# Kernel optimization log

Hardware: AMD Instinct MI355X
Metric: run time of the kernel (lower is better)

The kernel has to match this reference:

```python
import jax, jax.numpy as jnp
import numpy as np

N_HEAD = 16
D_K = 64
D_MODEL = N_HEAD * D_K
LN_EPS = 1e-5


def setup_inputs() -> dict:
    key = jax.random.key(0)
    ks = jax.random.split(key, 11)
    B, Tq, Tk = 4, 2048, 2048
    s = 1.0 / np.sqrt(D_MODEL)
    return {
        "q": jax.random.normal(ks[0], (B, Tq, D_MODEL), jnp.float32),
        "k": jax.random.normal(ks[1], (B, Tk, D_MODEL), jnp.float32),
        "v": jax.random.normal(ks[2], (B, Tk, D_MODEL), jnp.float32),
        "Wq": jax.random.normal(ks[3], (D_MODEL, D_MODEL), jnp.float32) * s,
        "bq": jnp.zeros((D_MODEL,), jnp.float32),
        "Wk": jax.random.normal(ks[4], (D_MODEL, D_MODEL), jnp.float32) * s,
        "bk": jnp.zeros((D_MODEL,), jnp.float32),
        "Wv": jax.random.normal(ks[5], (D_MODEL, D_MODEL), jnp.float32) * s,
        "bv": jnp.zeros((D_MODEL,), jnp.float32),
        "Wo": jax.random.normal(ks[6], (D_MODEL, D_MODEL), jnp.float32) * s,
        "bo": jnp.zeros((D_MODEL,), jnp.float32),
        "gamma": jnp.ones((D_MODEL,), jnp.float32),
        "beta": jnp.zeros((D_MODEL,), jnp.float32),
    }


def reference(q, k, v, Wq, bq, Wk, bk, Wv, bv, Wo, bo, gamma, beta):
    B, Tq, _ = q.shape
    Tk = k.shape[1]
    temperature = jnp.asarray(D_K ** 0.5, q.dtype)

    # projections (torch Linear: x @ W.T + b), reshape to heads: [B, T, H, DK]
    qh = (q @ Wq.T + bq).reshape(B, Tq, N_HEAD, D_K)
    kh = (k @ Wk.T + bk).reshape(B, Tk, N_HEAD, D_K)
    vh = (v @ Wv.T + bv).reshape(B, Tk, N_HEAD, D_K)

    # scores [B, H, Tq, Tk]; softmax over Tk (dropout is identity in eval)
    scores = jnp.einsum('bqhd,bkhd->bhqk', qh, kh) / temperature
    attn = jax.nn.softmax(scores, axis=-1)

    # attention output -> concat heads [B, Tq, D_MODEL]
    out = jnp.einsum('bhqk,bkhd->bqhd', attn, vh).reshape(B, Tq, D_MODEL)

    out = out @ Wo.T + bo
    x = out + q  # residual
    mu = jnp.mean(x, axis=-1, keepdims=True)
    var = jnp.var(x, axis=-1, keepdims=True)
    out_norm = (x - mu) * jax.lax.rsqrt(var + LN_EPS) * gamma + beta

    # attn returned in torch layout [NHead*B, Tq, Tk]
    attn_flat = attn.transpose(1, 0, 2, 3).reshape(N_HEAD * B, Tq, Tk)
    return (out_norm, attn_flat)
```

## Files before the change

### kernel.cpp

```cpp
#include <hip/hip_runtime.h>
#include <cstdint>
#include <cstddef>

typedef __attribute__((ext_vector_type(4))) float f32x4;
typedef __attribute__((ext_vector_type(8))) short s16x8;
typedef __attribute__((ext_vector_type(4))) unsigned short u16x4;
typedef __attribute__((ext_vector_type(8))) unsigned short u16x8;

#define MFMA16(a, b, c) __builtin_amdgcn_mfma_f32_16x16x32_bf16((a), (b), (c), 0, 0, 0)
#define GLOAD_LDS16(src, dst)                                             \
  __builtin_amdgcn_global_load_lds(                                       \
      (const __attribute__((address_space(1))) void*)(src),               \
      (__attribute__((address_space(3))) void*)(dst), 16, 0, 0)

static constexpr int kD = 1024;
static constexpr int kT = 2048;

__device__ __forceinline__ unsigned short f2bf(float f) {
  union { float f; uint32_t u; } v; v.f = f;
  uint32_t r = v.u + 0x7fffu + ((v.u >> 16) & 1u);
  return (unsigned short)(r >> 16);
}
__device__ __forceinline__ float bf2f(unsigned short h) {
  union { float f; uint32_t u; } v; v.u = ((uint32_t)h) << 16;
  return v.f;
}

__global__ __launch_bounds__(256) void convert_all_k(
    const float* __restrict__ q, const float* __restrict__ k,
    const float* __restrict__ v, const float* __restrict__ Wq,
    const float* __restrict__ Wk, const float* __restrict__ Wv,
    const float* __restrict__ Wo, unsigned short* __restrict__ q_hi,
    unsigned short* __restrict__ q_lo, unsigned short* __restrict__ k_hi,
    unsigned short* __restrict__ k_lo, unsigned short* __restrict__ v_b,
    unsigned short* __restrict__ Wq_hi, unsigned short* __restrict__ Wq_lo,
    unsigned short* __restrict__ Wk_hi, unsigned short* __restrict__ Wk_lo,
    unsigned short* __restrict__ Wv_b, unsigned short* __restrict__ Wo_b) {
  constexpr int nq4 = (4 * 2048 * 1024) / 4;
  constexpr int nw4 = (1024 * 1024) / 4;
  constexpr int total = 3 * nq4 + 4 * nw4;
  for (int i = blockIdx.x * 256 + threadIdx.x; i < total; i += gridDim.x * 256) {
    const float* src;
    unsigned short *hi, *lo = nullptr;
    int off;
    if (i < nq4) { src = q; hi = q_hi; lo = q_lo; off = i; }
    else if (i < 2 * nq4) { src = k; hi = k_hi; lo = k_lo; off = i - nq4; }
    else if (i < 3 * nq4) { src = v; hi = v_b; off = i - 2 * nq4; }
    else if (i < 3 * nq4 + nw4) { src = Wq; hi = Wq_hi; lo = Wq_lo; off = i - 3 * nq4; }
    else if (i < 3 * nq4 + 2 * nw4) { src = Wk; hi = Wk_hi; lo = Wk_lo; off = i - 3 * nq4 - nw4; }
    else if (i < 3 * nq4 + 3 * nw4) { src = Wv; hi = Wv_b; off = i - 3 * nq4 - 2 * nw4; }
    else { src = Wo; hi = Wo_b; off = i - 3 * nq4 - 3 * nw4; }
    f32x4 vv = ((const f32x4*)src)[off];
    u16x4 h4, l4;
#pragma unroll
    for (int j = 0; j < 4; j++) {
      h4[j] = f2bf(vv[j]);
      l4[j] = f2bf(vv[j] - bf2f(h4[j]));
    }
    ((u16x4*)hi)[off] = h4;
    if (lo) ((u16x4*)lo)[off] = l4;
  }
}

template <int MODE, int MINW>
__global__ __launch_bounds__(256, MINW) void gemm_bf16(
    const unsigned short* __restrict__ Xhi, const unsigned short* __restrict__ Xlo,
    const unsigned short* __restrict__ Whi, const unsigned short* __restrict__ Wlo,
    const float* __restrict__ bias, const float* __restrict__ resid,
    unsigned short* __restrict__ outB, float* __restrict__ outF, float oscale) {
  constexpr bool SPLIT = (MODE == 0);
  __shared__ unsigned short smem[(SPLIT ? 4 : 2) * 128 * 64];
  unsigned short* Ah = smem;
  unsigned short* Bh = smem + 8192;
  unsigned short* Al = SPLIT ? smem + 16384 : smem;
  unsigned short* Bl = SPLIT ? smem + 24576 : smem;

  const int tid = threadIdx.x, lane = tid & 63, w = tid >> 6;
  const int wg = (blockIdx.x & 7) * 64 + (blockIdx.x >> 3);
  const int m0 = (wg >> 3) * 128, n0 = (wg & 7) * 128;
  const int wm0 = (w >> 1) * 64, wn0 = (w & 1) * 64;
  const int lr = lane & 15, lk = lane >> 4;
  const int srow = lane >> 3, sslot = (lane & 7) ^ srow;

  const size_t xoff = (size_t)(m0 + w * 32 + srow) * kD + sslot * 8;
  const size_t woff = (size_t)(n0 + w * 32 + srow) * kD + sslot * 8;

  f32x4 acc[4][4];
#pragma unroll
  for (int i = 0; i < 4; i++)
#pragma unroll
    for (int j = 0; j < 4; j++) acc[i][j] = (f32x4){0.f, 0.f, 0.f, 0.f};

  for (int kt = 0; kt < kD / 64; ++kt) {
    __syncthreads();
    const int kof = kt * 64;
#pragma unroll
    for (int i = 0; i < 4; i++) {
      const int ldst = (w * 32 + i * 8) * 64;
      GLOAD_LDS16(Xhi + xoff + (size_t)i * 8 * kD + kof, &Ah[ldst]);
      GLOAD_LDS16(Whi + woff + (size_t)i * 8 * kD + kof, &Bh[ldst]);
      if constexpr (SPLIT) {
        GLOAD_LDS16(Xlo + xoff + (size_t)i * 8 * kD + kof, &Al[ldst]);
        GLOAD_LDS16(Wlo + woff + (size_t)i * 8 * kD + kof, &Bl[ldst]);
      }
    }
    __syncthreads();
#pragma unroll
    for (int ks = 0; ks < 2; ks++) {
      s16x8 af[4], bf[4], al[4], bl[4];
#pragma unroll
      for (int i = 0; i < 4; i++) {
        const int ra = wm0 + i * 16 + lr;
        const int oa = ra * 128 + ((((ks * 4) + lk) ^ (ra & 7)) << 4);
        const int rb = wn0 + i * 16 + lr;
        const int ob = rb * 128 + ((((ks * 4) + lk) ^ (rb & 7)) << 4);
        af[i] = *(const s16x8*)((const char*)Ah + oa);
        bf[i] = *(const s16x8*)((const char*)Bh + ob);
        if constexpr (SPLIT) {
          al[i] = *(const s16x8*)((const char*)Al + oa);
          bl[i] = *(const s16x8*)((const char*)Bl + ob);
        }
      }
#pragma unroll
      for (int i = 0; i < 4; i++)
#pragma unroll
        for (int j = 0; j < 4; j++) {
          if constexpr (SPLIT) {
            acc[i][j] = MFMA16(al[i], bf[j], acc[i][j]);
            acc[i][j] = MFMA16(af[i], bl[j], acc[i][j]);
          }
          acc[i][j] = MFMA16(af[i], bf[j], acc[i][j]);
        }
    }
  }

#pragma unroll
  for (int j = 0; j < 4; j++) {
    const int col = n0 + wn0 + j * 16 + lr;
    const float bv = bias[col];
#pragma unroll
    for (int i = 0; i < 4; i++)
#pragma unroll
      for (int r = 0; r < 4; r++) {
        const int row = m0 + wm0 + i * 16 + lk * 4 + r;
        const size_t idx = (size_t)row * kD + col;
        float vv = acc[i][j][r] + bv;
        if constexpr (MODE == 0) {
          outB[idx] = f2bf(vv * oscale);
        } else if constexpr (MODE == 1) {
          outB[idx] = f2bf(vv);
        } else {
          outF[idx] = vv + resid[idx];
        }
      }
  }
}

__global__ __launch_bounds__(256) void transpose_v(
    const unsigned short* __restrict__ vh, unsigned short* __restrict__ vhT) {
  __shared__ unsigned short lds[64 * 72];
  const int bx = blockIdx.x;
  const int tt = bx & 31, bhp = bx >> 5;
  const int b = bhp >> 4, h = bhp & 15;
  const int t0 = tt * 64, tid = threadIdx.x;
  {
    const int t = tid >> 2, c0 = (tid & 3) * 16;
    const unsigned short* src = &vh[(size_t)(b * kT + t0 + t) * kD + h * 64 + c0];
    u16x8 v0 = *(const u16x8*)src;
    u16x8 v1 = *(const u16x8*)(src + 8);
    *(u16x8*)&lds[t * 72 + c0] = v0;
    *(u16x8*)&lds[t * 72 + c0 + 8] = v1;
  }
  __syncthreads();
  {
    const int d = tid >> 2, tc0 = (tid & 3) * 16;
    u16x8 o0, o1;
#pragma unroll
    for (int i = 0; i < 8; i++) o0[i] = lds[(tc0 + i) * 72 + d];
#pragma unroll
    for (int i = 0; i < 8; i++) o1[i] = lds[(tc0 + 8 + i) * 72 + d];
    size_t base = ((size_t)((b * 16 + h) * 64 + d)) * kT + t0 + tc0;
    *(u16x8*)&vhT[base] = o0;
    *(u16x8*)&vhT[base + 8] = o1;
  }
}

__global__ __launch_bounds__(256, 2) void attn_fused(
    const unsigned short* __restrict__ qh, const unsigned short* __restrict__ kh,
    const unsigned short* __restrict__ vhT, unsigned short* __restrict__ attn_out,
    float* __restrict__ attn_p) {
  __shared__ unsigned short kbuf[2][64 * 64];
  __shared__ unsigned short vbuf[2][64 * 64];
  __shared__ unsigned short qp[9216];

  const int tid = threadIdx.x, lane = tid & 63, w = tid >> 6;
  const int lr = lane & 15, lk = lane >> 4;
  const int srow = lane >> 3, sslot = (lane & 7) ^ srow;
  const int wg = (blockIdx.x & 7) * 128 + (blockIdx.x >> 3);
  const int bh = wg >> 4, qt = wg & 15;
  const int h = bh >> 2, b = bh & 3;
  const int q0 = qt * 128, qm0 = w * 32;

  const size_t qsrc = (size_t)(b * kT + q0 + w * 32 + srow) * kD + h * 64 + sslot * 8;
#pragma unroll
  for (int i = 0; i < 4; i++)
    GLOAD_LDS16(qh + qsrc + (size_t)i * 8 * kD, &qp[(w * 32 + i * 8) * 64]);

  const size_t kbase = (size_t)(b * kT + w * 16 + srow) * kD + h * 64 + sslot * 8;
  const size_t vbase = ((size_t)((b * 16 + h) * 64) + w * 16 + srow) * kT + sslot * 8;

#pragma unroll
  for (int i = 0; i < 2; i++)
    GLOAD_LDS16(kh + kbase + (size_t)(i * 8) * kD, &kbuf[0][(w * 16 + i * 8) * 64]);
  __syncthreads();

  s16x8 qf[2][2];
#pragma unroll
  for (int mq = 0; mq < 2; mq++)
#pragma unroll
    for (int ks = 0; ks < 2; ks++) {
      const int rq = qm0 + mq * 16 + lr;
      qf[mq][ks] = *(const s16x8*)((const char*)qp + rq * 128 +
                                   ((((ks * 4) + lk) ^ (rq & 7)) << 4));
    }

  float l_part[2] = {0.f, 0.f};

  for (int kt = 0; kt < kT / 64; ++kt) {
    if (kt + 1 < kT / 64) {
#pragma unroll
      for (int i = 0; i < 2; i++)
        GLOAD_LDS16(kh + kbase + (size_t)((kt + 1) * 64 + i * 8) * kD,
                    &kbuf[(kt + 1) & 1][(w * 16 + i * 8) * 64]);
    }
    const unsigned short* kb = kbuf[kt & 1];
    f32x4 sc[2][4];
#pragma unroll
    for (int mq = 0; mq < 2; mq++)
#pragma unroll
      for (int ni = 0; ni < 4; ni++) sc[mq][ni] = (f32x4){0.f, 0.f, 0.f, 0.f};
#pragma unroll
    for (int ks = 0; ks < 2; ks++) {
      s16x8 kf[4];
#pragma unroll
      for (int ni = 0; ni < 4; ni++) {
        const int rk = ni * 16 + lr;
        kf[ni] = *(const s16x8*)((const char*)kb + rk * 128 +
                                 ((((ks * 4) + lk) ^ (rk & 7)) << 4));
      }
#pragma unroll
      for (int mq = 0; mq < 2; mq++)
#pragma unroll
        for (int ni = 0; ni < 4; ni++)
          sc[mq][ni] = MFMA16(kf[ni], qf[mq][ks], sc[mq][ni]);
    }
#pragma unroll
    for (int mq = 0; mq < 2; mq++)
#pragma unroll
      for (int ni = 0; ni < 4; ni++)
        l_part[mq] += __expf(sc[mq][ni][0]) + __expf(sc[mq][ni][1]) +
                      __expf(sc[mq][ni][2]) + __expf(sc[mq][ni][3]);
    __syncthreads();
  }

  float rl[2];
#pragma unroll
  for (int mq = 0; mq < 2; mq++) {
    float s = l_part[mq];
    s += __shfl_xor(s, 16, 64);
    s += __shfl_xor(s, 32, 64);
    rl[mq] = 1.0f / s;
  }

  f32x4 pv[2][4];
#pragma unroll
  for (int mq = 0; mq < 2; mq++)
#pragma unroll
    for (int nd = 0; nd < 4; nd++) pv[mq][nd] = (f32x4){0.f, 0.f, 0.f, 0.f};

#pragma unroll
  for (int i = 0; i < 2; i++) {
    const int ldst = (w * 16 + i * 8) * 64;
    GLOAD_LDS16(kh + kbase + (size_t)(i * 8) * kD, &kbuf[0][ldst]);
    GLOAD_LDS16(vhT + vbase + (size_t)i * 8 * kT, &vbuf[0][ldst]);
  }
  unsigned short* p_w = &qp[w * 2304];
  __syncthreads();

  for (int kt = 0; kt < kT / 64; ++kt) {
    if (kt + 1 < kT / 64) {
#pragma unroll
      for (int i = 0; i < 2; i++) {
        const int ldst = (w * 16 + i * 8) * 64;
        GLOAD_LDS16(kh + kbase + (size_t)((kt + 1) * 64 + i * 8) * kD,
                    &kbuf[(kt + 1) & 1][ldst]);
        GLOAD_LDS16(vhT + vbase + (size_t)i * 8 * kT + (kt + 1) * 64,
                    &vbuf[(kt + 1) & 1][ldst]);
      }
    }
    const unsigned short* kb = kbuf[kt & 1];
    const unsigned short* vb = vbuf[kt & 1];
    f32x4 sc[2][4];
#pragma unroll
    for (int mq = 0; mq < 2; mq++)
#pragma unroll
      for (int ni = 0; ni < 4; ni++) sc[mq][ni] = (f32x4){0.f, 0.f, 0.f, 0.f};
#pragma unroll
    for (int ks = 0; ks < 2; ks++) {
      s16x8 kf[4];
#pragma unroll
      for (int ni = 0; ni < 4; ni++) {
        const int rk = ni * 16 + lr;
        kf[ni] = *(const s16x8*)((const char*)kb + rk * 128 +
                                 ((((ks * 4) + lk) ^ (rk & 7)) << 4));
      }
#pragma unroll
      for (int mq = 0; mq < 2; mq++)
#pragma unroll
        for (int ni = 0; ni < 4; ni++)
          sc[mq][ni] = MFMA16(kf[ni], qf[mq][ks], sc[mq][ni]);
    }
#pragma unroll
    for (int mq = 0; mq < 2; mq++) {
      const int qrow = q0 + qm0 + mq * 16 + lr;
      float* prow = attn_p + ((size_t)(bh * kT + qrow)) * kT + kt * 64 + 4 * lk;
#pragma unroll
      for (int ni = 0; ni < 4; ni++) {
        f32x4 pr;
#pragma unroll
        for (int r = 0; r < 4; r++) pr[r] = __expf(sc[mq][ni][r]) * rl[mq];
        __builtin_nontemporal_store(pr, (f32x4*)(prow + ni * 16));
        uint32_t d0, d1;
        asm("v_cvt_pk_bf16_f32 %0, %1, %2" : "=v"(d0) : "v"(pr[0]), "v"(pr[1]));
        asm("v_cvt_pk_bf16_f32 %0, %1, %2" : "=v"(d1) : "v"(pr[2]), "v"(pr[3]));
        uint2 dd; dd.x = d0; dd.y = d1;
        *(uint2*)&p_w[(mq * 16 + lr) * 72 + ni * 16 + 4 * lk] = dd;
      }
    }
#pragma unroll
    for (int ks = 0; ks < 2; ks++) {
      s16x8 pf[2], vf[4];
#pragma unroll
      for (int mq = 0; mq < 2; mq++)
        pf[mq] = *(const s16x8*)&p_w[(mq * 16 + lr) * 72 + ks * 32 + lk * 8];
#pragma unroll
      for (int nd = 0; nd < 4; nd++) {
        const int row = nd * 16 + lr;
        const int sw2 = ((ks * 4) + lk) ^ (row & 7);
        vf[nd] = *(const s16x8*)((const char*)vb + row * 128 + (sw2 << 4));
      }
#pragma unroll
      for (int mq = 0; mq < 2; mq++)
#pragma unroll
        for (int nd = 0; nd < 4; nd++)
          pv[mq][nd] = MFMA16(pf[mq], vf[nd], pv[mq][nd]);
    }
    __syncthreads();
  }

#pragma unroll
  for (int mq = 0; mq < 2; mq++)
#pragma unroll
    for (int nd = 0; nd < 4; nd++)
#pragma unroll
      for (int r = 0; r < 4; r++) {
        const int qrow = q0 + qm0 + mq * 16 + lk * 4 + r;
        attn_out[((size_t)(b * kT + qrow)) * kD + h * 64 + nd * 16 + lr] =
            f2bf(pv[mq][nd][r]);
      }
}

__global__ __launch_bounds__(256) void ln_kernel(
    const float* __restrict__ x, const float* __restrict__ gamma,
    const float* __restrict__ beta, float* __restrict__ out) {
  __shared__ float ssum[4], ssq[4];
  const int row = blockIdx.x, tid = threadIdx.x;
  f32x4 v = *(const f32x4*)&x[(size_t)row * kD + tid * 4];
  float s = v[0] + v[1] + v[2] + v[3];
  float q2 = v[0] * v[0] + v[1] * v[1] + v[2] * v[2] + v[3] * v[3];
#pragma unroll
  for (int d = 1; d < 64; d <<= 1) {
    s += __shfl_xor(s, d, 64);
    q2 += __shfl_xor(q2, d, 64);
  }
  const int w = tid >> 6, lane = tid & 63;
  if (lane == 0) {
    ssum[w] = s;
    ssq[w] = q2;
  }
  __syncthreads();
  s = ssum[0] + ssum[1] + ssum[2] + ssum[3];
  q2 = ssq[0] + ssq[1] + ssq[2] + ssq[3];
  const float mu = s * (1.f / 1024.f);
  const float var = q2 * (1.f / 1024.f) - mu * mu;
  const float rstd = rsqrtf(var + 1e-5f);
  f32x4 g = *(const f32x4*)&gamma[tid * 4];
  f32x4 bb = *(const f32x4*)&beta[tid * 4];
  f32x4 o;
#pragma unroll
  for (int j = 0; j < 4; j++) o[j] = (v[j] - mu) * rstd * g[j] + bb[j];
  *(f32x4*)&out[(size_t)row * kD + tid * 4] = o;
}

extern "C" void kernel_launch(void* const* d_in, const int* in_sizes, int n_in,
                              void* d_out, int out_size, void* d_ws,
                              size_t ws_size, hipStream_t stream) {
  const float* q = (const float*)d_in[0];
  const float* k = (const float*)d_in[1];
  const float* v = (const float*)d_in[2];
  const float* Wq = (const float*)d_in[3];
  const float* bq = (const float*)d_in[4];
  const float* Wk = (const float*)d_in[5];
  const float* bk = (const float*)d_in[6];
  const float* Wv = (const float*)d_in[7];
  const float* bv = (const float*)d_in[8];
  const float* Wo = (const float*)d_in[9];
  const float* bo = (const float*)d_in[10];
  const float* gamma = (const float*)d_in[11];
  const float* beta = (const float*)d_in[12];

  float* out = (float*)d_out;
  float* attn_p = out + (size_t)8192 * 1024;

  constexpr size_t NQ = (size_t)4 * 2048 * 1024;
  constexpr size_t NW = (size_t)1024 * 1024;

  unsigned short* w16 = (unsigned short*)d_ws;
  unsigned short* q_hi = w16 + 0 * NQ;
  unsigned short* q_lo = w16 + 1 * NQ;
  unsigned short* k_hi = w16 + 2 * NQ;
  unsigned short* k_lo = w16 + 3 * NQ;
  unsigned short* v_b  = w16 + 4 * NQ;
  unsigned short* qh_b = w16 + 5 * NQ;
  unsigned short* kh_b = w16 + 6 * NQ;
  unsigned short* vh_b = w16 + 7 * NQ;
  unsigned short* vhT  = w16 + 8 * NQ;
  unsigned short* ao_b = w16 + 9 * NQ;
  unsigned short* Wq_hi = w16 + 10 * NQ;
  unsigned short* Wq_lo = Wq_hi + NW;
  unsigned short* Wk_hi = Wq_hi + 2 * NW;
  unsigned short* Wk_lo = Wq_hi + 3 * NW;
  unsigned short* Wv_b  = Wq_hi + 4 * NW;
  unsigned short* Wo_b  = Wq_hi + 5 * NW;
  float* xbuf = (float*)(Wq_hi + 6 * NW);

  dim3 blk(256);
  convert_all_k<<<2048, blk, 0, stream>>>(q, k, v, Wq, Wk, Wv, Wo, q_hi, q_lo,
                                          k_hi, k_lo, v_b, Wq_hi, Wq_lo, Wk_hi,
                                          Wk_lo, Wv_b, Wo_b);

  gemm_bf16<0, 2><<<512, blk, 0, stream>>>(q_hi, q_lo, Wq_hi, Wq_lo, bq, nullptr,
                                           qh_b, nullptr, 0.125f);
  gemm_bf16<0, 2><<<512, blk, 0, stream>>>(k_hi, k_lo, Wk_hi, Wk_lo, bk, nullptr,
                                           kh_b, nullptr, 1.0f);
  gemm_bf16<1, 3><<<512, blk, 0, stream>>>(v_b, nullptr, Wv_b, nullptr, bv, nullptr,
                                           vh_b, nullptr, 1.0f);
  transpose_v<<<2048, blk, 0, stream>>>(vh_b, vhT);
  attn_fused<<<1024, blk, 0, stream>>>(qh_b, kh_b, vhT, ao_b, attn_p);
  gemm_bf16<2, 3><<<512, blk, 0, stream>>>(ao_b, nullptr, Wo_b, nullptr, bo, q,
                                           nullptr, xbuf, 1.0f);
  ln_kernel<<<8192, blk, 0, stream>>>(xbuf, gamma, beta, out);
}
```

Before: 555.7 us.

## Replace split-bf16 Q/K projections with single-pass fp16 MFMA

The Q and K projections used a hi/lo bf16 split costing three MFMAs per tile plus extra conversion traffic and LDS. They now convert inputs and weights once to fp16, run one fp16 MFMA pass, and store qh/kh as fp16 so the QK^T scores in attention also use fp16 MFMA. This drops the lo buffers, halves projection MFMA work and cuts the bytes the convert kernel writes. Attention occupancy is raised to 3 waves. The trade-off is relying on fp16's extra mantissa bits instead of the split for score accuracy, with some overflow risk if activations are large.

```diff
diff --git a/kernel.cpp b/kernel.cpp
--- a/kernel.cpp
+++ b/kernel.cpp
@@ -4,10 +4,12 @@
 
 typedef __attribute__((ext_vector_type(4))) float f32x4;
 typedef __attribute__((ext_vector_type(8))) short s16x8;
+typedef __attribute__((ext_vector_type(8))) _Float16 f16x8;
 typedef __attribute__((ext_vector_type(4))) unsigned short u16x4;
 typedef __attribute__((ext_vector_type(8))) unsigned short u16x8;
 
-#define MFMA16(a, b, c) __builtin_amdgcn_mfma_f32_16x16x32_bf16((a), (b), (c), 0, 0, 0)
+#define MFMA_BF16(a, b, c) __builtin_amdgcn_mfma_f32_16x16x32_bf16((a), (b), (c), 0, 0, 0)
+#define MFMA_F16(a, b, c) __builtin_amdgcn_mfma_f32_16x16x32_f16((a), (b), (c), 0, 0, 0)
 #define GLOAD_LDS16(src, dst)                                             \
   __builtin_amdgcn_global_load_lds(                                       \
       (const __attribute__((address_space(1))) void*)(src),               \
@@ -21,59 +23,51 @@
   uint32_t r = v.u + 0x7fffu + ((v.u >> 16) & 1u);
   return (unsigned short)(r >> 16);
 }
-__device__ __forceinline__ float bf2f(unsigned short h) {
-  union { float f; uint32_t u; } v; v.u = ((uint32_t)h) << 16;
-  return v.f;
+__device__ __forceinline__ unsigned short f2h(float f) {
+  union { _Float16 h; unsigned short u; } cv;
+  cv.h = (_Float16)f;
+  return cv.u;
 }
 
 __global__ __launch_bounds__(256) void convert_all_k(
     const float* __restrict__ q, const float* __restrict__ k,
     const float* __restrict__ v, const float* __restrict__ Wq,
     const float* __restrict__ Wk, const float* __restrict__ Wv,
-    const float* __restrict__ Wo, unsigned short* __restrict__ q_hi,
-    unsigned short* __restrict__ q_lo, unsigned short* __restrict__ k_hi,
-    unsigned short* __restrict__ k_lo, unsigned short* __restrict__ v_b,
-    unsigned short* __restrict__ Wq_hi, unsigned short* __restrict__ Wq_lo,
-    unsigned short* __restrict__ Wk_hi, unsigned short* __restrict__ Wk_lo,
+    const float* __restrict__ Wo, unsigned short* __restrict__ q_h,
+    unsigned short* __restrict__ k_h, unsigned short* __restrict__ v_b,
+    unsigned short* __restrict__ Wq_h, unsigned short* __restrict__ Wk_h,
     unsigned short* __restrict__ Wv_b, unsigned short* __restrict__ Wo_b) {
   constexpr int nq4 = (4 * 2048 * 1024) / 4;
   constexpr int nw4 = (1024 * 1024) / 4;
   constexpr int total = 3 * nq4 + 4 * nw4;
   for (int i = blockIdx.x * 256 + threadIdx.x; i < total; i += gridDim.x * 256) {
     const float* src;
-    unsigned short *hi, *lo = nullptr;
+    unsigned short* dst;
     int off;
-    if (i < nq4) { src = q; hi = q_hi; lo = q_lo; off = i; }
-    else if (i < 2 * nq4) { src = k; hi = k_hi; lo = k_lo; off = i - nq4; }
-    else if (i < 3 * nq4) { src = v; hi = v_b; off = i - 2 * nq4; }
-    else if (i < 3 * nq4 + nw4) { src = Wq; hi = Wq_hi; lo = Wq_lo; off = i - 3 * nq4; }
-    else if (i < 3 * nq4 + 2 * nw4) { src = Wk; hi = Wk_hi; lo = Wk_lo; off = i - 3 * nq4 - nw4; }
-    else if (i < 3 * nq4 + 3 * nw4) { src = Wv; hi = Wv_b; off = i - 3 * nq4 - 2 * nw4; }
-    else { src = Wo; hi = Wo_b; off = i - 3 * nq4 - 3 * nw4; }
+    bool use_f16;
+    if (i < nq4) { src = q; dst = q_h; off = i; use_f16 = true; }
+    else if (i < 2 * nq4) { src = k; dst = k_h; off = i - nq4; use_f16 = true; }
+    else if (i < 3 * nq4) { src = v; dst = v_b; off = i - 2 * nq4; use_f16 = false; }
+    else if (i < 3 * nq4 + nw4) { src = Wq; dst = Wq_h; off = i - 3 * nq4; use_f16 = true; }
+    else if (i < 3 * nq4 + 2 * nw4) { src = Wk; dst = Wk_h; off = i - 3 * nq4 - nw4; use_f16 = true; }
+    else if (i < 3 * nq4 + 3 * nw4) { src = Wv; dst = Wv_b; off = i - 3 * nq4 - 2 * nw4; use_f16 = false; }
+    else { src = Wo; dst = Wo_b; off = i - 3 * nq4 - 3 * nw4; use_f16 = false; }
     f32x4 vv = ((const f32x4*)src)[off];
-    u16x4 h4, l4;
-#pragma unroll
-    for (int j = 0; j < 4; j++) {
-      h4[j] = f2bf(vv[j]);
-      l4[j] = f2bf(vv[j] - bf2f(h4[j]));
-    }
-    ((u16x4*)hi)[off] = h4;
-    if (lo) ((u16x4*)lo)[off] = l4;
-  }
-}
-
-template <int MODE, int MINW>
-__global__ __launch_bounds__(256, MINW) void gemm_bf16(
-    const unsigned short* __restrict__ Xhi, const unsigned short* __restrict__ Xlo,
-    const unsigned short* __restrict__ Whi, const unsigned short* __restrict__ Wlo,
+    u16x4 o4;
+#pragma unroll
+    for (int j = 0; j < 4; j++) o4[j] = use_f16 ? f2h(vv[j]) : f2bf(vv[j]);
+    ((u16x4*)dst)[off] = o4;
+  }
+}
+
+template <int MODE>
+__global__ __launch_bounds__(256, 3) void gemm_16(
+    const unsigned short* __restrict__ X, const unsigned short* __restrict__ W,
     const float* __restrict__ bias, const float* __restrict__ resid,
     unsigned short* __restrict__ outB, float* __restrict__ outF, float oscale) {
-  constexpr bool SPLIT = (MODE == 0);
-  __shared__ unsigned short smem[(SPLIT ? 4 : 2) * 128 * 64];
+  __shared__ unsigned short smem[2 * 128 * 64];
   unsigned short* Ah = smem;
   unsigned short* Bh = smem + 8192;
-  unsigned short* Al = SPLIT ? smem + 16384 : smem;
-  unsigned short* Bl = SPLIT ? smem + 24576 : smem;
 
   const int tid = threadIdx.x, lane = tid & 63, w = tid >> 6;
   const int wg = (blockIdx.x & 7) * 64 + (blockIdx.x >> 3);
@@ -97,17 +91,13 @@
 #pragma unroll
     for (int i = 0; i < 4; i++) {
       const int ldst = (w * 32 + i * 8) * 64;
-      GLOAD_LDS16(Xhi + xoff + (size_t)i * 8 * kD + kof, &Ah[ldst]);
-      GLOAD_LDS16(Whi + woff + (size_t)i * 8 * kD + kof, &Bh[ldst]);
-      if constexpr (SPLIT) {
-        GLOAD_LDS16(Xlo + xoff + (size_t)i * 8 * kD + kof, &Al[ldst]);
-        GLOAD_LDS16(Wlo + woff + (size_t)i * 8 * kD + kof, &Bl[ldst]);
-      }
+      GLOAD_LDS16(X + xoff + (size_t)i * 8 * kD + kof, &Ah[ldst]);
+      GLOAD_LDS16(W + woff + (size_t)i * 8 * kD + kof, &Bh[ldst]);
     }
     __syncthreads();
 #pragma unroll
     for (int ks = 0; ks < 2; ks++) {
-      s16x8 af[4], bf[4], al[4], bl[4];
+      s16x8 af[4], bf[4];
 #pragma unroll
       for (int i = 0; i < 4; i++) {
         const int ra = wm0 + i * 16 + lr;
@@ -116,20 +106,17 @@
         const int ob = rb * 128 + ((((ks * 4) + lk) ^ (rb & 7)) << 4);
         af[i] = *(const s16x8*)((const char*)Ah + oa);
         bf[i] = *(const s16x8*)((const char*)Bh + ob);
-        if constexpr (SPLIT) {
-          al[i] = *(const s16x8*)((const char*)Al + oa);
-          bl[i] = *(const s16x8*)((const char*)Bl + ob);
-        }
       }
 #pragma unroll
       for (int i = 0; i < 4; i++)
 #pragma unroll
         for (int j = 0; j < 4; j++) {
-          if constexpr (SPLIT) {
-            acc[i][j] = MFMA16(al[i], bf[j], acc[i][j]);
-            acc[i][j] = MFMA16(af[i], bl[j], acc[i][j]);
+          if constexpr (MODE == 0) {
+            acc[i][j] = MFMA_F16(*(const f16x8*)&af[i], *(const f16x8*)&bf[j],
+                                 acc[i][j]);
+          } else {
+            acc[i][j] = MFMA_BF16(af[i], bf[j], acc[i][j]);
           }
-          acc[i][j] = MFMA16(af[i], bf[j], acc[i][j]);
         }
     }
   }
@@ -146,7 +133,7 @@
         const size_t idx = (size_t)row * kD + col;
         float vv = acc[i][j][r] + bv;
         if constexpr (MODE == 0) {
-          outB[idx] = f2bf(vv * oscale);
+          outB[idx] = f2h(vv * oscale);
         } else if constexpr (MODE == 1) {
           outB[idx] = f2bf(vv);
         } else {
@@ -185,7 +172,7 @@
   }
 }
 
-__global__ __launch_bounds__(256, 2) void attn_fused(
+__global__ __launch_bounds__(256, 3) void attn_fused(
     const unsigned short* __restrict__ qh, const unsigned short* __restrict__ kh,
     const unsigned short* __restrict__ vhT, unsigned short* __restrict__ attn_out,
     float* __restrict__ attn_p) {
@@ -214,13 +201,13 @@
     GLOAD_LDS16(kh + kbase + (size_t)(i * 8) * kD, &kbuf[0][(w * 16 + i * 8) * 64]);
   __syncthreads();
 
-  s16x8 qf[2][2];
+  f16x8 qf[2][2];
 #pragma unroll
   for (int mq = 0; mq < 2; mq++)
 #pragma unroll
     for (int ks = 0; ks < 2; ks++) {
       const int rq = qm0 + mq * 16 + lr;
-      qf[mq][ks] = *(const s16x8*)((const char*)qp + rq * 128 +
+      qf[mq][ks] = *(const f16x8*)((const char*)qp + rq * 128 +
                                    ((((ks * 4) + lk) ^ (rq & 7)) << 4));
     }
 
@@ -241,18 +228,18 @@
       for (int ni = 0; ni < 4; ni++) sc[mq][ni] = (f32x4){0.f, 0.f, 0.f, 0.f};
 #pragma unroll
     for (int ks = 0; ks < 2; ks++) {
-      s16x8 kf[4];
+      f16x8 kf[4];
 #pragma unroll
       for (int ni = 0; ni < 4; ni++) {
         const int rk = ni * 16 + lr;
-        kf[ni] = *(const s16x8*)((const char*)kb + rk * 128 +
+        kf[ni] = *(const f16x8*)((const char*)kb + rk * 128 +
                                  ((((ks * 4) + lk) ^ (rk & 7)) << 4));
       }
 #pragma unroll
       for (int mq = 0; mq < 2; mq++)
 #pragma unroll
         for (int ni = 0; ni < 4; ni++)
-          sc[mq][ni] = MFMA16(kf[ni], qf[mq][ks], sc[mq][ni]);
+          sc[mq][ni] = MFMA_F16(kf[ni], qf[mq][ks], sc[mq][ni]);
     }
 #pragma unroll
     for (int mq = 0; mq < 2; mq++)
@@ -307,18 +294,18 @@
       for (int ni = 0; ni < 4; ni++) sc[mq][ni] = (f32x4){0.f, 0.f, 0.f, 0.f};
 #pragma unroll
     for (int ks = 0; ks < 2; ks++) {
-      s16x8 kf[4];
+      f16x8 kf[4];
 #pragma unroll
       for (int ni = 0; ni < 4; ni++) {
         const int rk = ni * 16 + lr;
-        kf[ni] = *(const s16x8*)((const char*)kb + rk * 128 +
+        kf[ni] = *(const f16x8*)((const char*)kb + rk * 128 +
                                  ((((ks * 4) + lk) ^ (rk & 7)) << 4));
       }
 #pragma unroll
       for (int mq = 0; mq < 2; mq++)
 #pragma unroll
         for (int ni = 0; ni < 4; ni++)
-          sc[mq][ni] = MFMA16(kf[ni], qf[mq][ks], sc[mq][ni]);
+          sc[mq][ni] = MFMA_F16(kf[ni], qf[mq][ks], sc[mq][ni]);
     }
 #pragma unroll
     for (int mq = 0; mq < 2; mq++) {
@@ -353,7 +340,7 @@
       for (int mq = 0; mq < 2; mq++)
 #pragma unroll
         for (int nd = 0; nd < 4; nd++)
-          pv[mq][nd] = MFMA16(pf[mq], vf[nd], pv[mq][nd]);
+          pv[mq][nd] = MFMA_BF16(pf[mq], vf[nd], pv[mq][nd]);
     }
     __syncthreads();
   }
@@ -426,38 +413,32 @@
   constexpr size_t NW = (size_t)1024 * 1024;
 
   unsigned short* w16 = (unsigned short*)d_ws;
-  unsigned short* q_hi = w16 + 0 * NQ;
-  unsigned short* q_lo = w16 + 1 * NQ;
-  unsigned short* k_hi = w16 + 2 * NQ;
-  unsigned short* k_lo = w16 + 3 * NQ;
-  unsigned short* v_b  = w16 + 4 * NQ;
-  unsigned short* qh_b = w16 + 5 * NQ;
-  unsigned short* kh_b = w16 + 6 * NQ;
-  unsigned short* vh_b = w16 + 7 * NQ;
-  unsigned short* vhT  = w16 + 8 * NQ;
-  unsigned short* ao_b = w16 + 9 * NQ;
-  unsigned short* Wq_hi = w16 + 10 * NQ;
-  unsigned short* Wq_lo = Wq_hi + NW;
-  unsigned short* Wk_hi = Wq_hi + 2 * NW;
-  unsigned short* Wk_lo = Wq_hi + 3 * NW;
-  unsigned short* Wv_b  = Wq_hi + 4 * NW;
-  unsigned short* Wo_b  = Wq_hi + 5 * NW;
-  float* xbuf = (float*)(Wq_hi + 6 * NW);
+  unsigned short* q_h  = w16 + 0 * NQ;
+  unsigned short* k_h  = w16 + 1 * NQ;
+  unsigned short* v_b  = w16 + 2 * NQ;
+  unsigned short* qh_h = w16 + 3 * NQ;
+  unsigned short* kh_h = w16 + 4 * NQ;
+  unsigned short* vh_b = w16 + 5 * NQ;
+  unsigned short* vhT  = w16 + 6 * NQ;
+  unsigned short* ao_b = w16 + 7 * NQ;
+  unsigned short* Wq_h = w16 + 8 * NQ;
+  unsigned short* Wk_h = Wq_h + NW;
+  unsigned short* Wv_b = Wq_h + 2 * NW;
+  unsigned short* Wo_b = Wq_h + 3 * NW;
+  float* xbuf = (float*)(Wq_h + 4 * NW);
 
   dim3 blk(256);
-  convert_all_k<<<2048, blk, 0, stream>>>(q, k, v, Wq, Wk, Wv, Wo, q_hi, q_lo,
-                                          k_hi, k_lo, v_b, Wq_hi, Wq_lo, Wk_hi,
-                                          Wk_lo, Wv_b, Wo_b);
-
-  gemm_bf16<0, 2><<<512, blk, 0, stream>>>(q_hi, q_lo, Wq_hi, Wq_lo, bq, nullptr,
-                                           qh_b, nullptr, 0.125f);
-  gemm_bf16<0, 2><<<512, blk, 0, stream>>>(k_hi, k_lo, Wk_hi, Wk_lo, bk, nullptr,
-                                           kh_b, nullptr, 1.0f);
-  gemm_bf16<1, 3><<<512, blk, 0, stream>>>(v_b, nullptr, Wv_b, nullptr, bv, nullptr,
-                                           vh_b, nullptr, 1.0f);
+  convert_all_k<<<2048, blk, 0, stream>>>(q, k, v, Wq, Wk, Wv, Wo, q_h, k_h,
+                                          v_b, Wq_h, Wk_h, Wv_b, Wo_b);
+
+  gemm_16<0><<<512, blk, 0, stream>>>(q_h, Wq_h, bq, nullptr, qh_h, nullptr,
+                                      0.125f);
+  gemm_16<0><<<512, blk, 0, stream>>>(k_h, Wk_h, bk, nullptr, kh_h, nullptr,
+                                      1.0f);
+  gemm_16<1><<<512, blk, 0, stream>>>(v_b, Wv_b, bv, nullptr, vh_b, nullptr,
+                                      1.0f);
   transpose_v<<<2048, blk, 0, stream>>>(vh_b, vhT);
-  attn_fused<<<1024, blk, 0, stream>>>(qh_b, kh_b, vhT, ao_b, attn_p);
-  gemm_bf16<2, 3><<<512, blk, 0, stream>>>(ao_b, nullptr, Wo_b, nullptr, bo, q,
-                                           nullptr, xbuf, 1.0f);
+  attn_fused<<<1024, blk, 0, stream>>>(qh_h, kh_h, vhT, ao_b, attn_p);
+  gemm_16<2><<<512, blk, 0, stream>>>(ao_b, Wo_b, bo, q, nullptr, xbuf, 1.0f);
   ln_kernel<<<8192, blk, 0, stream>>>(xbuf, gamma, beta, out);
 }
```

Measured after the change: 506.2 us. 1.1x faster.
